# Kernel tuning notes

Hardware: AMD Instinct MI355X
Metric: run time of the kernel (lower is better)

The kernel has to match this reference:

```python
import jax, jax.numpy as jnp
import numpy as np
import math

B, N, DIM, H, DH, NNULL = 2, 2048, 1024, 16, 64, 2
SCALE = 8.0
LN_EPS = 1e-5


def _alibi_slopes(heads):
    # heads is a power of 2 here (16): slopes = start * start**i
    start = 2.0 ** (-(2.0 ** (-(math.log2(heads) - 3))))
    return np.array([start * (start ** i) for i in range(heads)], dtype=np.float32)


def setup_inputs() -> dict:
    key = jax.random.key(0)
    ks = jax.random.split(key, 6)
    inner = H * DH
    return {
        "x": jax.random.normal(ks[0], (B, N, DIM), dtype=jnp.float32),
        "norm_g": jnp.ones((DIM,), jnp.float32),
        "norm_b": jnp.zeros((DIM,), jnp.float32),
        "Wq": jax.random.normal(ks[1], (DIM, inner), jnp.float32) * 0.02,
        "Wkv": jax.random.normal(ks[2], (DIM, 2 * inner), jnp.float32) * 0.02,
        "q_scale": jnp.ones((DH,), jnp.float32),
        "k_scale": jnp.ones((DH,), jnp.float32),
        "null_kv": jax.random.normal(ks[3], (H, 2 * NNULL, DH), jnp.float32),
        "Wout": jax.random.normal(ks[4], (inner, DIM), jnp.float32) * 0.02,
    }


def _l2norm(t):
    # matches F.normalize: x / max(||x||, 1e-12)
    n = jnp.sqrt(jnp.sum(t * t, axis=-1, keepdims=True))
    return t / jnp.maximum(n, 1e-12)


def reference(x, norm_g, norm_b, Wq, Wkv, q_scale, k_scale, null_kv, Wout):
    b, n, dim = x.shape
    h, dh, nn = H, DH, NNULL
    j = n + nn

    # NOTE: faithful to source -- K/V come from the PRE-norm x (kv_input bound
    # before x = self.norm(x)); only Q uses the LayerNorm'd x.
    mu = jnp.mean(x, axis=-1, keepdims=True)
    var = jnp.mean((x - mu) ** 2, axis=-1, keepdims=True)
    xn = (x - mu) * jax.lax.rsqrt(var + LN_EPS) * norm_g + norm_b

    q = (xn @ Wq).reshape(b, n, h, dh).transpose(0, 2, 1, 3)          # b h n d
    kv = x @ Wkv
    k, v = jnp.split(kv, 2, axis=-1)
    k = k.reshape(b, n, h, dh).transpose(0, 2, 1, 3)                   # b h n d
    v = v.reshape(b, n, h, dh).transpose(0, 2, 1, 3)

    # null kv: (h, 2*nn, dh) -> (h, nn, 2, dh)
    null = null_kv.reshape(h, nn, 2, dh)
    nk = jnp.broadcast_to(null[:, :, 0, :][None], (b, h, nn, dh))
    nv = jnp.broadcast_to(null[:, :, 1, :][None], (b, h, nn, dh))
    k = jnp.concatenate([nk, k], axis=2)                               # b h j d
    v = jnp.concatenate([nv, v], axis=2)

    q = _l2norm(q) * q_scale
    k = _l2norm(k) * k_scale

    sim = jnp.einsum('bhid,bhjd->bhij', q, k) * SCALE                  # b h n j

    # ALiBi bias: rows at positions j-n..j-1, cols 0..j-1
    irow = jnp.arange(j - n, j)
    jcol = jnp.arange(j)
    bias = -jnp.abs(jcol[None, :] - irow[:, None]).astype(sim.dtype)   # (n, j)
    slopes = jnp.asarray(_alibi_slopes(h))[:, None, None]              # (h,1,1)
    sim = sim + slopes * bias

    # causal mask: triu with offset j - n + 1 (null kv always visible)
    causal = jnp.triu(jnp.ones((n, j), dtype=bool), k=j - n + 1)
    neg = jnp.finfo(sim.dtype).max
    sim = jnp.where(causal[None, None], -neg, sim)

    attn = jax.nn.softmax(sim, axis=-1)
    out = jnp.einsum('bhij,bhjd->bhid', attn, v)
    out = out.transpose(0, 2, 1, 3).reshape(b, n, h * dh)
    return out @ Wout
```

## Files before the change

### kernel.cpp

```cpp
#include <hip/hip_runtime.h>
#include <hip/hip_bf16.h>
#include <stdint.h>

#define H_    16
#define N_    2048
#define DIM_  1024
#define DH_   64
#define NN_   2
#define J_    2050
#define JP_   2112
#define B_    2
#define M_    4096
#define NSEG_ 84

#define S8L_  11.541560327111707f
#define LOG2E_ 1.4426950408889634f

typedef unsigned short u16;
typedef unsigned int u32;
typedef short bf16x8 __attribute__((ext_vector_type(8)));
typedef float f32x4 __attribute__((ext_vector_type(4)));

__device__ __forceinline__ u16 f2b(float f) {
  union { float f; unsigned int i; } v; v.f = f;
  unsigned int r = v.i + 0x7fffu + ((v.i >> 16) & 1u);
  return (u16)(r >> 16);
}
__device__ __forceinline__ float b2f(u16 u) {
  union { unsigned int i; float f; } v; v.i = ((unsigned int)u) << 16; return v.f;
}
__device__ __forceinline__ float lo2f(u32 u) {
  union { u32 i; float f; } v; v.i = u << 16; return v.f;
}
__device__ __forceinline__ float hi2f(u32 u) {
  union { u32 i; float f; } v; v.i = u & 0xffff0000u; return v.f;
}
__device__ __forceinline__ void unp8(const uint4 u, float* d) {
  d[0] = lo2f(u.x); d[1] = hi2f(u.x); d[2] = lo2f(u.y); d[3] = hi2f(u.y);
  d[4] = lo2f(u.z); d[5] = hi2f(u.z); d[6] = lo2f(u.w); d[7] = hi2f(u.w);
}
__device__ __forceinline__ u32 pk2(float a, float b) {
  union { __hip_bfloat162 h; u32 u; } x;
  x.h = __float22bfloat162_rn(make_float2(a, b));
  return x.u;
}
__device__ __forceinline__ void dma16(const u16* g, u16* l) {
  __builtin_amdgcn_global_load_lds(
      (const __attribute__((address_space(1))) u32*)(const void*)g,
      (__attribute__((address_space(3))) u32*)(void*)l, 16, 0, 0);
}

__global__ __launch_bounds__(256) void ktranspose3(const float* __restrict__ Wq,
                                                   const float* __restrict__ Wkv,
                                                   const float* __restrict__ Wout,
                                                   u16* __restrict__ WqT,
                                                   u16* __restrict__ WkvT,
                                                   u16* __restrict__ WoutT) {
  __shared__ float tile[32][33];
  int bx = blockIdx.x;
  const float* in; u16* out; int C; int cx;
  if (bx < 32)      { in = Wq;   out = WqT;   C = 1024; cx = bx; }
  else if (bx < 96) { in = Wkv;  out = WkvT;  C = 2048; cx = bx - 32; }
  else              { in = Wout; out = WoutT; C = 1024; cx = bx - 96; }
  const int R = 1024;
  int tx = threadIdx.x & 31, ty = threadIdx.x >> 5;
  int c0 = cx * 32, r0 = blockIdx.y * 32;
  #pragma unroll
  for (int i = 0; i < 32; i += 8)
    tile[ty + i][tx] = in[(size_t)(r0 + ty + i) * C + c0 + tx];
  __syncthreads();
  #pragma unroll
  for (int i = 0; i < 32; i += 8)
    out[(size_t)(c0 + ty + i) * R + r0 + tx] = f2b(tile[tx][ty + i]);
}

__global__ __launch_bounds__(256) void lnorm_k(const float* __restrict__ x,
                                               const float* __restrict__ g,
                                               const float* __restrict__ bb,
                                               u16* __restrict__ xn,
                                               u16* __restrict__ xbf) {
  int row = blockIdx.x;
  int t = threadIdx.x;
  float4 rw = *(const float4*)(x + (size_t)row * DIM_ + t * 4);
  float v0 = rw.x, v1 = rw.y, v2 = rw.z, v3 = rw.w;
  uint2 cw;
  cw.x = pk2(v0, v1);
  cw.y = pk2(v2, v3);
  *(uint2*)(xbf + (size_t)row * DIM_ + t * 4) = cw;
  float s = v0 + v1 + v2 + v3;
  float ss = v0 * v0 + v1 * v1 + v2 * v2 + v3 * v3;
  #pragma unroll
  for (int o = 32; o; o >>= 1) { s += __shfl_xor(s, o, 64); ss += __shfl_xor(ss, o, 64); }
  __shared__ float red[8];
  int lane = t & 63, w = t >> 6;
  if (lane == 0) { red[w] = s; red[4 + w] = ss; }
  __syncthreads();
  float S = red[0] + red[1] + red[2] + red[3];
  float SS = red[4] + red[5] + red[6] + red[7];
  float mu = S * (1.0f / DIM_);
  float var = SS * (1.0f / DIM_) - mu * mu;
  float rs = rsqrtf(var + 1e-5f);
  float4 gv = *(const float4*)(g + t * 4);
  float4 bv = *(const float4*)(bb + t * 4);
  uint2 ow;
  ow.x = pk2((v0 - mu) * rs * gv.x + bv.x, (v1 - mu) * rs * gv.y + bv.y);
  ow.y = pk2((v2 - mu) * rs * gv.z + bv.z, (v3 - mu) * rs * gv.w + bv.w);
  *(uint2*)(xn + (size_t)row * DIM_ + t * 4) = ow;
}

template <int MODE>
__global__ __launch_bounds__(256) void gemm_k(const u16* __restrict__ A,
                                              const u16* __restrict__ BT,
                                              void* __restrict__ dst0,
                                              void* __restrict__ dst1,
                                              const float* __restrict__ scale,
                                              int M, int Nc, int K) {
  __shared__ u16 As[2][128 * 64];
  __shared__ u16 Bs[2][64 * 64];
  int tid = threadIdx.x, wv = tid >> 6, lane = tid & 63;
  int fm = lane & 15, fg = lane >> 4;
  int nlin = (int)blockIdx.x + (int)gridDim.x * (int)blockIdx.y;
  int gx = (int)gridDim.x;
  int ypc = (int)gridDim.y >> 3;
  int mm = nlin >> 3;
  int row0 = ((nlin & 7) * ypc + mm / gx) * 128;
  int col0 = (mm % gx) * 64;
  f32x4 acc[2][4] = {};
  int srow = lane >> 3;
  int skb = ((lane & 7) ^ srow) * 8;
  const u16* Ag = A + (size_t)(row0 + wv * 32 + srow) * K + skb;
  const u16* Bg = BT + (size_t)(col0 + wv * 16 + srow) * K + skb;
  int fr7 = fm & 7;
  int ak0 = (fg ^ fr7) * 8;
  int ak1 = ((fg + 4) ^ fr7) * 8;
  {
    u16* AsW = As[0] + (wv * 32) * 64;
    u16* BsW = Bs[0] + (wv * 16) * 64;
    dma16(Ag,                    AsW);
    dma16(Ag + (size_t)8 * K,    AsW + 8 * 64);
    dma16(Ag + (size_t)16 * K,   AsW + 16 * 64);
    dma16(Ag + (size_t)24 * K,   AsW + 24 * 64);
    dma16(Bg,                    BsW);
    dma16(Bg + (size_t)8 * K,    BsW + 8 * 64);
  }
  __syncthreads();
  int cur = 0;
  for (int k0 = 0; k0 < K; k0 += 64) {
    if (k0 + 64 < K) {
      int kn = k0 + 64;
      u16* AsW = As[cur ^ 1] + (wv * 32) * 64;
      u16* BsW = Bs[cur ^ 1] + (wv * 16) * 64;
      dma16(Ag + kn,                    AsW);
      dma16(Ag + (size_t)8 * K + kn,    AsW + 8 * 64);
      dma16(Ag + (size_t)16 * K + kn,   AsW + 16 * 64);
      dma16(Ag + (size_t)24 * K + kn,   AsW + 24 * 64);
      dma16(Bg + kn,                    BsW);
      dma16(Bg + (size_t)8 * K + kn,    BsW + 8 * 64);
    }
    bf16x8 af0[2], af1[2], bf0[4], bf1[4];
    #pragma unroll
    for (int mt = 0; mt < 2; mt++) {
      int rbase = (wv * 32 + mt * 16 + fm) * 64;
      af0[mt] = *(const bf16x8*)&As[cur][rbase + ak0];
      af1[mt] = *(const bf16x8*)&As[cur][rbase + ak1];
    }
    #pragma unroll
    for (int nt = 0; nt < 4; nt++) {
      int rbase = (nt * 16 + fm) * 64;
      bf0[nt] = *(const bf16x8*)&Bs[cur][rbase + ak0];
      bf1[nt] = *(const bf16x8*)&Bs[cur][rbase + ak1];
    }
    #pragma unroll
    for (int mt = 0; mt < 2; mt++)
      #pragma unroll
      for (int nt = 0; nt < 4; nt++) {
        acc[mt][nt] = __builtin_amdgcn_mfma_f32_16x16x32_bf16(af0[mt], bf0[nt], acc[mt][nt], 0, 0, 0);
        acc[mt][nt] = __builtin_amdgcn_mfma_f32_16x16x32_bf16(af1[mt], bf1[nt], acc[mt][nt], 0, 0, 0);
      }
    __syncthreads();
    cur ^= 1;
  }
  if (MODE == 1) {
    float* C = (float*)dst0;
    #pragma unroll
    for (int mt = 0; mt < 2; mt++)
      #pragma unroll
      for (int r = 0; r < 4; r++) {
        int m = row0 + wv * 32 + mt * 16 + fg * 4 + r;
        #pragma unroll
        for (int nt = 0; nt < 4; nt++)
          C[(size_t)m * Nc + col0 + nt * 16 + fm] = acc[mt][nt][r];
      }
  } else {
    bool isK = (MODE == 2) || (col0 < 1024);
    int h = (isK ? col0 : col0 - 1024) >> 6;
    float sv[4];
    if (isK) {
      #pragma unroll
      for (int nt = 0; nt < 4; nt++) sv[nt] = scale[nt * 16 + fm];
      if (MODE == 2) {
        #pragma unroll
        for (int nt = 0; nt < 4; nt++) sv[nt] *= S8L_;
      }
    }
    u16* Do = (u16*)((MODE == 3 && !isK) ? dst1 : dst0);
    #pragma unroll
    for (int mt = 0; mt < 2; mt++) {
      #pragma unroll
      for (int r = 0; r < 4; r++) {
        float inv = 1.0f;
        if (isK) {
          float ssp = 0.0f;
          #pragma unroll
          for (int nt = 0; nt < 4; nt++) ssp += acc[mt][nt][r] * acc[mt][nt][r];
          #pragma unroll
          for (int o = 1; o <= 8; o <<= 1) ssp += __shfl_xor(ssp, o, 64);
          inv = 1.0f / fmaxf(sqrtf(ssp), 1e-12f);
        }
        int m = row0 + wv * 32 + mt * 16 + fg * 4 + r;
        int b = m >> 11, n = m & 2047;
        size_t base;
        if (MODE == 2)      base = (((size_t)(b * H_ + h)) * N_ + n) * 64;
        else if (isK)       base = (((size_t)(b * H_ + h)) * JP_ + (n + NN_)) * 64;
        else                base = (((size_t)(b * H_ + h)) * J_ + (n + NN_)) * 64;
        #pragma unroll
        for (int nt = 0; nt < 4; nt++) {
          float val = acc[mt][nt][r];
          if (isK) val = val * inv * sv[nt];
          Do[base + nt * 16 + fm] = f2b(val);
        }
      }
    }
  }
}

__global__ __launch_bounds__(256) void vtransp_k(const u16* __restrict__ Vb,
                                                 const float* __restrict__ nkv,
                                                 const float* __restrict__ ks,
                                                 u16* __restrict__ Kb,
                                                 u16* __restrict__ VTp) {
  __shared__ u16 tile[64][80];
  int t = threadIdx.x;
  int c = blockIdx.x, bh = blockIdx.y, h = bh & 15;
  int jl = t >> 2, dc = (t & 3) * 16;
  int j = c * 64 + jl;
  if (j < NN_) {
    float kvv[16];
    float kssp = 0.0f;
    #pragma unroll
    for (int e = 0; e < 16; e++) {
      float vv = nkv[(size_t)(h * 4 + 2 * j + 1) * 64 + dc + e];
      tile[jl][dc + e] = f2b(vv);
      float kv = nkv[(size_t)(h * 4 + 2 * j) * 64 + dc + e];
      kvv[e] = kv; kssp += kv * kv;
    }
    kssp += __shfl_xor(kssp, 1, 64);
    kssp += __shfl_xor(kssp, 2, 64);
    float inv = 1.0f / fmaxf(sqrtf(kssp), 1e-12f);
    #pragma unroll
    for (int e = 0; e < 16; e++)
      Kb[((size_t)bh * JP_ + j) * 64 + dc + e] = f2b(kvv[e] * inv * ks[dc + e]);
  } else if (j < J_) {
    const uint4* src = (const uint4*)(Vb + ((size_t)bh * J_ + j) * 64 + dc);
    *(uint4*)&tile[jl][dc] = src[0];
    *(uint4*)&tile[jl][dc + 8] = src[1];
  } else {
    uint4 z = {0, 0, 0, 0};
    *(uint4*)&tile[jl][dc] = z;
    *(uint4*)&tile[jl][dc + 8] = z;
    uint4* kd = (uint4*)(Kb + ((size_t)bh * JP_ + j) * 64 + dc);
    kd[0] = z;
    kd[1] = z;
  }
  __syncthreads();
  int d = t >> 2, p0 = (t & 3) * 16;
  u16 tmp[16] __attribute__((aligned(16)));
  #pragma unroll
  for (int e = 0; e < 16; e++) {
    int pos = p0 + e;
    int h2 = pos >> 5, rem = pos & 31;
    int fgp = rem >> 3, tt = rem & 7;
    int nt = tt >> 2, r = tt & 3;
    int jloc = (h2 * 2 + nt) * 16 + fgp * 4 + r;
    tmp[e] = tile[jloc][d];
  }
  uint4* dstp = (uint4*)(VTp + ((size_t)bh * 64 + d) * JP_ + c * 64 + p0);
  dstp[0] = ((uint4*)tmp)[0];
  dstp[1] = ((uint4*)tmp)[1];
}

__global__ __launch_bounds__(256, 6) void attn_k(const u16* __restrict__ Qn,
                                                 const u16* __restrict__ Kb,
                                                 const u16* __restrict__ VTp,
                                                 const float* __restrict__ qs,
                                                 const float* __restrict__ ks,
                                                 u16* __restrict__ partials) {
  __shared__ u16 Ks0[64 * 32], Ks1[64 * 32];
  __shared__ u16 Vs0[64 * 32], Vs1[64 * 32];
  int tid = threadIdx.x;
  int wv = tid >> 6, lane = tid & 63;
  int fm = lane & 15, fg = lane >> 4;
  int n = (int)blockIdx.x + NSEG_ * (int)blockIdx.y;
  int m = n >> 3;
  int bh = (n & 7) * 4 + m / NSEG_;
  int segid = m % NSEG_;
  int h = bh & 15;
  int cum = 0, qt = 0, seg = 0;
  #pragma unroll 1
  for (int i = 0; i < 32; i++) {
    int t = 31 - i, s = (t + 9) >> 3;
    if (segid < cum + s) { qt = t; seg = segid - cum; break; }
    cum += s;
  }
  int q0 = qt * 64;
  int q = q0 + wv * 16 + fm;
  float slope = exp2f(-0.5f * (float)(h + 1));
  float prod = fabsf(qs[lane] * ks[lane]);
  #pragma unroll
  for (int o = 32; o; o >>= 1) prod = fmaxf(prod, __shfl_xor(prod, o, 64));
  float MbL = 8.0f * prod * LOG2E_;
  float slopeL = slope * LOG2E_;
  const u16* qp = Qn + ((size_t)bh * N_ + q) * 64 + fg * 8;
  bf16x8 qf0 = *(const bf16x8*)(qp);
  bf16x8 qf1 = *(const bf16x8*)(qp + 32);
  f32x4 accO[4] = {};
  float lp = 0.0f;
  int lr = lane >> 2;
  int kbs = ((lane & 3) ^ ((lane >> 3) & 3)) * 8;
  int fs = (fg ^ ((fm >> 1) & 3)) * 8;
  const u16* KbBH = Kb + (size_t)bh * JP_ * 64;
  const u16* VTbh = VTp + (size_t)bh * 64 * JP_;
  int c0 = seg * 8;
  int c1 = min(c0 + 8, qt + 2);
  float bias0 = slopeL * (float)(c0 * 64 + fg * 4 - q - 2) - MbL;
  float sr1 = slopeL, sr2 = slopeL * 2.0f, sr3 = slopeL * 3.0f;
  float s16 = slopeL * 16.0f;
  float d64 = slopeL * 64.0f;
  for (int c = c0; c < c1; c++) {
    int jb = c * 64;
    __syncthreads();
    const u16* Kg = KbBH + (size_t)(jb + wv * 16 + lr) * 64 + kbs;
    dma16(Kg,      Ks0 + wv * 512);
    dma16(Kg + 32, Ks1 + wv * 512);
    const u16* Vg = VTbh + (size_t)(wv * 16 + lr) * JP_ + jb + kbs;
    dma16(Vg,      Vs0 + wv * 512);
    dma16(Vg + 32, Vs1 + wv * 512);
    __syncthreads();
    f32x4 accS[4] = {};
    #pragma unroll
    for (int nt = 0; nt < 4; nt++) {
      bf16x8 kf0 = *(const bf16x8*)&Ks0[(nt * 16 + fm) * 32 + fs];
      accS[nt] = __builtin_amdgcn_mfma_f32_16x16x32_bf16(kf0, qf0, accS[nt], 0, 0, 0);
      bf16x8 kf1 = *(const bf16x8*)&Ks1[(nt * 16 + fm) * 32 + fs];
      accS[nt] = __builtin_amdgcn_mfma_f32_16x16x32_bf16(kf1, qf1, accS[nt], 0, 0, 0);
    }
    union { bf16x8 v; u32 u[4]; } P0, P1;
    float lps = 0.0f;
    float bnt = bias0;
    if (c < qt) {
      #pragma unroll
      for (int nt = 0; nt < 4; nt++) {
        float e0 = __builtin_amdgcn_exp2f(accS[nt][0] + bnt);
        float e1 = __builtin_amdgcn_exp2f((accS[nt][1] + sr1) + bnt);
        float e2 = __builtin_amdgcn_exp2f((accS[nt][2] + sr2) + bnt);
        float e3 = __builtin_amdgcn_exp2f((accS[nt][3] + sr3) + bnt);
        u32 w0 = pk2(e0, e1);
        u32 w1 = pk2(e2, e3);
        lps += (e0 + e1) + (e2 + e3);
        if (nt < 2) { P0.u[nt * 2] = w0; P0.u[nt * 2 + 1] = w1; }
        else        { P1.u[(nt - 2) * 2] = w0; P1.u[(nt - 2) * 2 + 1] = w1; }
        bnt += s16;
      }
    } else {
      int thr = q + 2 - jb;
      #pragma unroll
      for (int nt = 0; nt < 4; nt++) {
        int ib = nt * 16 + fg * 4;
        float e0 = __builtin_amdgcn_exp2f(accS[nt][0] + bnt);
        float e1 = __builtin_amdgcn_exp2f((accS[nt][1] + sr1) + bnt);
        float e2 = __builtin_amdgcn_exp2f((accS[nt][2] + sr2) + bnt);
        float e3 = __builtin_amdgcn_exp2f((accS[nt][3] + sr3) + bnt);
        e0 = (ib + 0 <= thr) ? e0 : 0.0f;
        e1 = (ib + 1 <= thr) ? e1 : 0.0f;
        e2 = (ib + 2 <= thr) ? e2 : 0.0f;
        e3 = (ib + 3 <= thr) ? e3 : 0.0f;
        u32 w0 = pk2(e0, e1);
        u32 w1 = pk2(e2, e3);
        lps += (e0 + e1) + (e2 + e3);
        if (nt < 2) { P0.u[nt * 2] = w0; P0.u[nt * 2 + 1] = w1; }
        else        { P1.u[(nt - 2) * 2] = w0; P1.u[(nt - 2) * 2 + 1] = w1; }
        bnt += s16;
      }
    }
    lp += lps;
    bias0 += d64;
    #pragma unroll
    for (int nt = 0; nt < 4; nt++) {
      bf16x8 vf0 = *(const bf16x8*)&Vs0[(nt * 16 + fm) * 32 + fs];
      accO[nt] = __builtin_amdgcn_mfma_f32_16x16x32_bf16(vf0, P0.v, accO[nt], 0, 0, 0);
      bf16x8 vf1 = *(const bf16x8*)&Vs1[(nt * 16 + fm) * 32 + fs];
      accO[nt] = __builtin_amdgcn_mfma_f32_16x16x32_bf16(vf1, P1.v, accO[nt], 0, 0, 0);
    }
  }
  lp += __shfl_xor(lp, 16, 64);
  lp += __shfl_xor(lp, 32, 64);
  u16* P = partials + ((size_t)bh * NSEG_ + segid) * 4224;
  int sq = wv * 16 + fm;
  #pragma unroll
  for (int nt = 0; nt < 4; nt++) {
    uint2 ow;
    ow.x = pk2(accO[nt][0], accO[nt][1]);
    ow.y = pk2(accO[nt][2], accO[nt][3]);
    *(uint2*)(P + sq * 64 + nt * 16 + fg * 4) = ow;
  }
  if (fg == 0) *(float*)(P + 4096 + 2 * sq) = lp;
}

__global__ __launch_bounds__(256) void comb_k(const u16* __restrict__ partials,
                                              u16* __restrict__ AO) {
  int qt = blockIdx.x, bh = blockIdx.y, b = bh >> 4, h = bh & 15;
  int t = threadIdx.x, q = t >> 2, dq = (t & 3) * 16;
  int s = (qt + 9) >> 3;
  int cum = 0;
  for (int tt = qt + 1; tt < 32; tt++) cum += (tt + 9) >> 3;
  float acc[16] = {};
  float lsum = 0.0f;
  for (int k = 0; k < s; k++) {
    const u16* P = partials + ((size_t)bh * NSEG_ + cum + k) * 4224;
    uint4 a = *(const uint4*)(P + q * 64 + dq);
    uint4 bq = *(const uint4*)(P + q * 64 + dq + 8);
    float tmp[8];
    unp8(a, tmp);
    #pragma unroll
    for (int e = 0; e < 8; e++) acc[e] += tmp[e];
    unp8(bq, tmp);
    #pragma unroll
    for (int e = 0; e < 8; e++) acc[8 + e] += tmp[e];
    lsum += *(const float*)(P + 4096 + 2 * q);
  }
  float linv = 1.0f / lsum;
  int n = qt * 64 + q;
  u16* dst = AO + (((size_t)(b * N_ + n)) * H_ + h) * 64 + dq;
  u16 ov[16] __attribute__((aligned(16)));
  #pragma unroll
  for (int e = 0; e < 16; e++) ov[e] = f2b(acc[e] * linv);
  *(uint4*)dst = ((uint4*)ov)[0];
  *(uint4*)(dst + 8) = ((uint4*)ov)[1];
}

extern "C" void kernel_launch(void* const* d_in, const int* in_sizes, int n_in,
                              void* d_out, int out_size, void* d_ws, size_t ws_size,
                              hipStream_t stream) {
  const float* x    = (const float*)d_in[0];
  const float* ng   = (const float*)d_in[1];
  const float* nb   = (const float*)d_in[2];
  const float* Wq   = (const float*)d_in[3];
  const float* Wkv  = (const float*)d_in[4];
  const float* qs   = (const float*)d_in[5];
  const float* ks   = (const float*)d_in[6];
  const float* nkv  = (const float*)d_in[7];
  const float* Wout = (const float*)d_in[8];
  float* out = (float*)d_out;
  char* ws = (char*)d_ws;

  u16* xn    = (u16*)(ws + 0);
  u16* WoutT = (u16*)(ws + 8388608);
  u16* Qn    = (u16*)(ws + 10485760);
  u16* Kb    = (u16*)(ws + 18874368);
  u16* VTp   = (u16*)(ws + 27525120);
  u16* xbf   = (u16*)(ws + 36175872);
  u16* WqT   = (u16*)(ws + 44564480);
  u16* WkvT  = (u16*)(ws + 46661632);
  u16* Vb    = (u16*)(ws + 50855936);
  u16* parts = xbf;
  u16* AO    = xn;

  ktranspose3<<<dim3(128, 32), 256, 0, stream>>>(Wq, Wkv, Wout, WqT, WkvT, WoutT);
  lnorm_k<<<4096, 256, 0, stream>>>(x, ng, nb, xn, xbf);
  gemm_k<2><<<dim3(16, 32), 256, 0, stream>>>(xn, WqT, Qn, nullptr, qs, M_, 1024, 1024);
  gemm_k<3><<<dim3(32, 32), 256, 0, stream>>>(xbf, WkvT, Kb, Vb, ks, M_, 2048, 1024);
  vtransp_k<<<dim3(33, 32), 256, 0, stream>>>(Vb, nkv, ks, Kb, VTp);
  attn_k<<<dim3(NSEG_, 32), 256, 0, stream>>>(Qn, Kb, VTp, qs, ks, parts);
  comb_k<<<dim3(32, 32), 256, 0, stream>>>(parts, AO);
  gemm_k<1><<<dim3(16, 32), 256, 0, stream>>>(AO, WoutT, out, nullptr, nullptr, M_, 1024, 1024);
}
```

Before: 214.4 us.

## Double query tile per attention block to 128 rows, reusing K/V fragments

Each wave now processes 32 query rows (two 16-row MFMA tiles) instead of 16, so every K/V tile loaded into shared memory and every K/V fragment read from LDS feeds twice as many MFMAs. Segments are re-split into 9-chunk pieces over 128-row query tiles, and the partial-combine kernel is updated to the new slot layout. Waves whose rows lie entirely above the causal diagonal of a chunk skip compute. The cost is roughly doubled accumulator registers (occupancy hint lowered from 6 to 4), fewer blocks for load balance, and more masked work on the diagonal.

```diff
diff --git a/kernel.cpp b/kernel.cpp
--- a/kernel.cpp
+++ b/kernel.cpp
@@ -11,7 +11,9 @@
 #define JP_   2112
 #define B_    2
 #define M_    4096
-#define NSEG_ 84
+#define QT2_  16
+#define NSEG2_ 39
+#define SLOT2_ 8448
 
 #define S8L_  11.541560327111707f
 #define LOG2E_ 1.4426950408889634f
@@ -25,9 +27,6 @@
   union { float f; unsigned int i; } v; v.f = f;
   unsigned int r = v.i + 0x7fffu + ((v.i >> 16) & 1u);
   return (u16)(r >> 16);
-}
-__device__ __forceinline__ float b2f(u16 u) {
-  union { unsigned int i; float f; } v; v.i = ((unsigned int)u) << 16; return v.f;
 }
 __device__ __forceinline__ float lo2f(u32 u) {
   union { u32 i; float f; } v; v.i = u << 16; return v.f;
@@ -289,7 +288,44 @@
   dstp[1] = ((uint4*)tmp)[1];
 }
 
-__global__ __launch_bounds__(256, 6) void attn_k(const u16* __restrict__ Qn,
+#define SOFTMAX16(ACCS, BSTART, FULLVIS, THR, LP, PW)                                \
+  {                                                                                  \
+    float bnt = (BSTART);                                                            \
+    float lps = 0.0f;                                                                \
+    if (FULLVIS) {                                                                   \
+      _Pragma("unroll")                                                              \
+      for (int nt = 0; nt < 4; nt++) {                                               \
+        float e0 = __builtin_amdgcn_exp2f(ACCS[nt][0] + bnt);                        \
+        float e1 = __builtin_amdgcn_exp2f((ACCS[nt][1] + sr1) + bnt);                \
+        float e2 = __builtin_amdgcn_exp2f((ACCS[nt][2] + sr2) + bnt);                \
+        float e3 = __builtin_amdgcn_exp2f((ACCS[nt][3] + sr3) + bnt);                \
+        PW[nt * 2] = pk2(e0, e1);                                                    \
+        PW[nt * 2 + 1] = pk2(e2, e3);                                                \
+        lps += (e0 + e1) + (e2 + e3);                                                \
+        bnt += s16;                                                                  \
+      }                                                                              \
+    } else {                                                                         \
+      _Pragma("unroll")                                                              \
+      for (int nt = 0; nt < 4; nt++) {                                               \
+        int ib = nt * 16 + fg4;                                                      \
+        float e0 = __builtin_amdgcn_exp2f(ACCS[nt][0] + bnt);                        \
+        float e1 = __builtin_amdgcn_exp2f((ACCS[nt][1] + sr1) + bnt);                \
+        float e2 = __builtin_amdgcn_exp2f((ACCS[nt][2] + sr2) + bnt);                \
+        float e3 = __builtin_amdgcn_exp2f((ACCS[nt][3] + sr3) + bnt);                \
+        e0 = (ib + 0 <= (THR)) ? e0 : 0.0f;                                          \
+        e1 = (ib + 1 <= (THR)) ? e1 : 0.0f;                                          \
+        e2 = (ib + 2 <= (THR)) ? e2 : 0.0f;                                          \
+        e3 = (ib + 3 <= (THR)) ? e3 : 0.0f;                                          \
+        PW[nt * 2] = pk2(e0, e1);                                                    \
+        PW[nt * 2 + 1] = pk2(e2, e3);                                                \
+        lps += (e0 + e1) + (e2 + e3);                                                \
+        bnt += s16;                                                                  \
+      }                                                                              \
+    }                                                                                \
+    LP += lps;                                                                       \
+  }
+
+__global__ __launch_bounds__(256, 4) void attn_k(const u16* __restrict__ Qn,
                                                  const u16* __restrict__ Kb,
                                                  const u16* __restrict__ VTp,
                                                  const float* __restrict__ qs,
@@ -300,39 +336,43 @@
   int tid = threadIdx.x;
   int wv = tid >> 6, lane = tid & 63;
   int fm = lane & 15, fg = lane >> 4;
-  int n = (int)blockIdx.x + NSEG_ * (int)blockIdx.y;
+  int fg4 = fg * 4;
+  int n = (int)blockIdx.x + NSEG2_ * (int)blockIdx.y;
   int m = n >> 3;
-  int bh = (n & 7) * 4 + m / NSEG_;
-  int segid = m % NSEG_;
+  int bh = (n & 7) * 4 + m / NSEG2_;
+  int segid = m % NSEG2_;
   int h = bh & 15;
-  int cum = 0, qt = 0, seg = 0;
+  int cum = 0, qt2 = 0, seg = 0;
   #pragma unroll 1
-  for (int i = 0; i < 32; i++) {
-    int t = 31 - i, s = (t + 9) >> 3;
-    if (segid < cum + s) { qt = t; seg = segid - cum; break; }
+  for (int i = 0; i < 16; i++) {
+    int t = 15 - i, s = (2 * t + 11) / 9;
+    if (segid < cum + s) { qt2 = t; seg = segid - cum; break; }
     cum += s;
   }
-  int q0 = qt * 64;
-  int q = q0 + wv * 16 + fm;
+  int q0 = qt2 * 128;
+  int qw = q0 + wv * 32;
+  int qr = qw + fm;
   float slope = exp2f(-0.5f * (float)(h + 1));
   float prod = fabsf(qs[lane] * ks[lane]);
   #pragma unroll
   for (int o = 32; o; o >>= 1) prod = fmaxf(prod, __shfl_xor(prod, o, 64));
   float MbL = 8.0f * prod * LOG2E_;
   float slopeL = slope * LOG2E_;
-  const u16* qp = Qn + ((size_t)bh * N_ + q) * 64 + fg * 8;
-  bf16x8 qf0 = *(const bf16x8*)(qp);
-  bf16x8 qf1 = *(const bf16x8*)(qp + 32);
-  f32x4 accO[4] = {};
-  float lp = 0.0f;
+  const u16* qp = Qn + ((size_t)bh * N_ + qr) * 64 + fg * 8;
+  bf16x8 qa0 = *(const bf16x8*)(qp);
+  bf16x8 qa1 = *(const bf16x8*)(qp + 32);
+  bf16x8 qb0 = *(const bf16x8*)(qp + 16 * 64);
+  bf16x8 qb1 = *(const bf16x8*)(qp + 16 * 64 + 32);
+  f32x4 accO[2][4] = {};
+  float lp0 = 0.0f, lp1 = 0.0f;
   int lr = lane >> 2;
   int kbs = ((lane & 3) ^ ((lane >> 3) & 3)) * 8;
   int fs = (fg ^ ((fm >> 1) & 3)) * 8;
   const u16* KbBH = Kb + (size_t)bh * JP_ * 64;
   const u16* VTbh = VTp + (size_t)bh * 64 * JP_;
-  int c0 = seg * 8;
-  int c1 = min(c0 + 8, qt + 2);
-  float bias0 = slopeL * (float)(c0 * 64 + fg * 4 - q - 2) - MbL;
+  int c0 = seg * 9;
+  int c1 = min(c0 + 9, 2 * qt2 + 3);
+  float bias0 = slopeL * (float)(c0 * 64 + fg4 - qr - 2) - MbL;
   float sr1 = slopeL, sr2 = slopeL * 2.0f, sr3 = slopeL * 3.0f;
   float s16 = slopeL * 16.0f;
   float d64 = slopeL * 64.0f;
@@ -346,106 +386,84 @@
     dma16(Vg,      Vs0 + wv * 512);
     dma16(Vg + 32, Vs1 + wv * 512);
     __syncthreads();
-    f32x4 accS[4] = {};
+    if (jb <= qw + 33) {
+      f32x4 accS0[4] = {}, accS1[4] = {};
+      #pragma unroll
+      for (int nt = 0; nt < 4; nt++) {
+        bf16x8 kf0 = *(const bf16x8*)&Ks0[(nt * 16 + fm) * 32 + fs];
+        accS0[nt] = __builtin_amdgcn_mfma_f32_16x16x32_bf16(kf0, qa0, accS0[nt], 0, 0, 0);
+        accS1[nt] = __builtin_amdgcn_mfma_f32_16x16x32_bf16(kf0, qb0, accS1[nt], 0, 0, 0);
+        bf16x8 kf1 = *(const bf16x8*)&Ks1[(nt * 16 + fm) * 32 + fs];
+        accS0[nt] = __builtin_amdgcn_mfma_f32_16x16x32_bf16(kf1, qa1, accS0[nt], 0, 0, 0);
+        accS1[nt] = __builtin_amdgcn_mfma_f32_16x16x32_bf16(kf1, qb1, accS1[nt], 0, 0, 0);
+      }
+      union { bf16x8 v[2]; u32 u[8]; } PA, PB;
+      bool fv0 = (jb + 61 <= qw);
+      bool fv1 = (jb + 61 <= qw + 16);
+      int thr0 = qr + 2 - jb;
+      SOFTMAX16(accS0, bias0, fv0, thr0, lp0, PA.u);
+      SOFTMAX16(accS1, bias0 - s16, fv1, thr0 + 16, lp1, PB.u);
+      #pragma unroll
+      for (int nt = 0; nt < 4; nt++) {
+        bf16x8 vf0 = *(const bf16x8*)&Vs0[(nt * 16 + fm) * 32 + fs];
+        accO[0][nt] = __builtin_amdgcn_mfma_f32_16x16x32_bf16(vf0, PA.v[0], accO[0][nt], 0, 0, 0);
+        accO[1][nt] = __builtin_amdgcn_mfma_f32_16x16x32_bf16(vf0, PB.v[0], accO[1][nt], 0, 0, 0);
+        bf16x8 vf1 = *(const bf16x8*)&Vs1[(nt * 16 + fm) * 32 + fs];
+        accO[0][nt] = __builtin_amdgcn_mfma_f32_16x16x32_bf16(vf1, PA.v[1], accO[0][nt], 0, 0, 0);
+        accO[1][nt] = __builtin_amdgcn_mfma_f32_16x16x32_bf16(vf1, PB.v[1], accO[1][nt], 0, 0, 0);
+      }
+    }
+    bias0 += d64;
+  }
+  lp0 += __shfl_xor(lp0, 16, 64);
+  lp0 += __shfl_xor(lp0, 32, 64);
+  lp1 += __shfl_xor(lp1, 16, 64);
+  lp1 += __shfl_xor(lp1, 32, 64);
+  u16* P = partials + ((size_t)bh * NSEG2_ + segid) * SLOT2_;
+  #pragma unroll
+  for (int mt = 0; mt < 2; mt++) {
+    int sq = wv * 32 + mt * 16 + fm;
     #pragma unroll
     for (int nt = 0; nt < 4; nt++) {
-      bf16x8 kf0 = *(const bf16x8*)&Ks0[(nt * 16 + fm) * 32 + fs];
-      accS[nt] = __builtin_amdgcn_mfma_f32_16x16x32_bf16(kf0, qf0, accS[nt], 0, 0, 0);
-      bf16x8 kf1 = *(const bf16x8*)&Ks1[(nt * 16 + fm) * 32 + fs];
-      accS[nt] = __builtin_amdgcn_mfma_f32_16x16x32_bf16(kf1, qf1, accS[nt], 0, 0, 0);
-    }
-    union { bf16x8 v; u32 u[4]; } P0, P1;
-    float lps = 0.0f;
-    float bnt = bias0;
-    if (c < qt) {
-      #pragma unroll
-      for (int nt = 0; nt < 4; nt++) {
-        float e0 = __builtin_amdgcn_exp2f(accS[nt][0] + bnt);
-        float e1 = __builtin_amdgcn_exp2f((accS[nt][1] + sr1) + bnt);
-        float e2 = __builtin_amdgcn_exp2f((accS[nt][2] + sr2) + bnt);
-        float e3 = __builtin_amdgcn_exp2f((accS[nt][3] + sr3) + bnt);
-        u32 w0 = pk2(e0, e1);
-        u32 w1 = pk2(e2, e3);
-        lps += (e0 + e1) + (e2 + e3);
-        if (nt < 2) { P0.u[nt * 2] = w0; P0.u[nt * 2 + 1] = w1; }
-        else        { P1.u[(nt - 2) * 2] = w0; P1.u[(nt - 2) * 2 + 1] = w1; }
-        bnt += s16;
-      }
-    } else {
-      int thr = q + 2 - jb;
-      #pragma unroll
-      for (int nt = 0; nt < 4; nt++) {
-        int ib = nt * 16 + fg * 4;
-        float e0 = __builtin_amdgcn_exp2f(accS[nt][0] + bnt);
-        float e1 = __builtin_amdgcn_exp2f((accS[nt][1] + sr1) + bnt);
-        float e2 = __builtin_amdgcn_exp2f((accS[nt][2] + sr2) + bnt);
-        float e3 = __builtin_amdgcn_exp2f((accS[nt][3] + sr3) + bnt);
-        e0 = (ib + 0 <= thr) ? e0 : 0.0f;
-        e1 = (ib + 1 <= thr) ? e1 : 0.0f;
-        e2 = (ib + 2 <= thr) ? e2 : 0.0f;
-        e3 = (ib + 3 <= thr) ? e3 : 0.0f;
-        u32 w0 = pk2(e0, e1);
-        u32 w1 = pk2(e2, e3);
-        lps += (e0 + e1) + (e2 + e3);
-        if (nt < 2) { P0.u[nt * 2] = w0; P0.u[nt * 2 + 1] = w1; }
-        else        { P1.u[(nt - 2) * 2] = w0; P1.u[(nt - 2) * 2 + 1] = w1; }
-        bnt += s16;
-      }
-    }
-    lp += lps;
-    bias0 += d64;
-    #pragma unroll
-    for (int nt = 0; nt < 4; nt++) {
-      bf16x8 vf0 = *(const bf16x8*)&Vs0[(nt * 16 + fm) * 32 + fs];
-      accO[nt] = __builtin_amdgcn_mfma_f32_16x16x32_bf16(vf0, P0.v, accO[nt], 0, 0, 0);
-      bf16x8 vf1 = *(const bf16x8*)&Vs1[(nt * 16 + fm) * 32 + fs];
-      accO[nt] = __builtin_amdgcn_mfma_f32_16x16x32_bf16(vf1, P1.v, accO[nt], 0, 0, 0);
-    }
-  }
-  lp += __shfl_xor(lp, 16, 64);
-  lp += __shfl_xor(lp, 32, 64);
-  u16* P = partials + ((size_t)bh * NSEG_ + segid) * 4224;
-  int sq = wv * 16 + fm;
-  #pragma unroll
-  for (int nt = 0; nt < 4; nt++) {
-    uint2 ow;
-    ow.x = pk2(accO[nt][0], accO[nt][1]);
-    ow.y = pk2(accO[nt][2], accO[nt][3]);
-    *(uint2*)(P + sq * 64 + nt * 16 + fg * 4) = ow;
-  }
-  if (fg == 0) *(float*)(P + 4096 + 2 * sq) = lp;
+      uint2 ow;
+      ow.x = pk2(accO[mt][nt][0], accO[mt][nt][1]);
+      ow.y = pk2(accO[mt][nt][2], accO[mt][nt][3]);
+      *(uint2*)(P + sq * 64 + nt * 16 + fg4) = ow;
+    }
+    if (fg == 0) *(float*)(P + 8192 + 2 * sq) = (mt == 0) ? lp0 : lp1;
+  }
 }
 
 __global__ __launch_bounds__(256) void comb_k(const u16* __restrict__ partials,
                                               u16* __restrict__ AO) {
-  int qt = blockIdx.x, bh = blockIdx.y, b = bh >> 4, h = bh & 15;
-  int t = threadIdx.x, q = t >> 2, dq = (t & 3) * 16;
-  int s = (qt + 9) >> 3;
+  int qt2 = blockIdx.x, bh = blockIdx.y, b = bh >> 4, h = bh & 15;
+  int t = threadIdx.x, q = t >> 1, dh = (t & 1) * 32;
+  int s = (2 * qt2 + 11) / 9;
   int cum = 0;
-  for (int tt = qt + 1; tt < 32; tt++) cum += (tt + 9) >> 3;
-  float acc[16] = {};
+  for (int tt = qt2 + 1; tt < 16; tt++) cum += (2 * tt + 11) / 9;
+  float acc[32] = {};
   float lsum = 0.0f;
   for (int k = 0; k < s; k++) {
-    const u16* P = partials + ((size_t)bh * NSEG_ + cum + k) * 4224;
-    uint4 a = *(const uint4*)(P + q * 64 + dq);
-    uint4 bq = *(const uint4*)(P + q * 64 + dq + 8);
+    const u16* P = partials + ((size_t)bh * NSEG2_ + cum + k) * SLOT2_;
     float tmp[8];
-    unp8(a, tmp);
-    #pragma unroll
-    for (int e = 0; e < 8; e++) acc[e] += tmp[e];
-    unp8(bq, tmp);
-    #pragma unroll
-    for (int e = 0; e < 8; e++) acc[8 + e] += tmp[e];
-    lsum += *(const float*)(P + 4096 + 2 * q);
+    #pragma unroll
+    for (int w = 0; w < 4; w++) {
+      uint4 a = *(const uint4*)(P + q * 64 + dh + w * 8);
+      unp8(a, tmp);
+      #pragma unroll
+      for (int e = 0; e < 8; e++) acc[w * 8 + e] += tmp[e];
+    }
+    lsum += *(const float*)(P + 8192 + 2 * q);
   }
   float linv = 1.0f / lsum;
-  int n = qt * 64 + q;
-  u16* dst = AO + (((size_t)(b * N_ + n)) * H_ + h) * 64 + dq;
-  u16 ov[16] __attribute__((aligned(16)));
-  #pragma unroll
-  for (int e = 0; e < 16; e++) ov[e] = f2b(acc[e] * linv);
-  *(uint4*)dst = ((uint4*)ov)[0];
-  *(uint4*)(dst + 8) = ((uint4*)ov)[1];
+  int nrow = qt2 * 128 + q;
+  u16* dst = AO + (((size_t)(b * N_ + nrow)) * H_ + h) * 64 + dh;
+  u16 ov[32] __attribute__((aligned(16)));
+  #pragma unroll
+  for (int e = 0; e < 32; e++) ov[e] = f2b(acc[e] * linv);
+  #pragma unroll
+  for (int w = 0; w < 4; w++)
+    *(uint4*)(dst + w * 8) = ((uint4*)ov)[w];
 }
 
 extern "C" void kernel_launch(void* const* d_in, const int* in_sizes, int n_in,
@@ -480,7 +498,7 @@
   gemm_k<2><<<dim3(16, 32), 256, 0, stream>>>(xn, WqT, Qn, nullptr, qs, M_, 1024, 1024);
   gemm_k<3><<<dim3(32, 32), 256, 0, stream>>>(xbf, WkvT, Kb, Vb, ks, M_, 2048, 1024);
   vtransp_k<<<dim3(33, 32), 256, 0, stream>>>(Vb, nkv, ks, Kb, VTp);
-  attn_k<<<dim3(NSEG_, 32), 256, 0, stream>>>(Qn, Kb, VTp, qs, ks, parts);
-  comb_k<<<dim3(32, 32), 256, 0, stream>>>(parts, AO);
+  attn_k<<<dim3(NSEG2_, 32), 256, 0, stream>>>(Qn, Kb, VTp, qs, ks, parts);
+  comb_k<<<dim3(16, 32), 256, 0, stream>>>(parts, AO);
   gemm_k<1><<<dim3(16, 32), 256, 0, stream>>>(AO, WoutT, out, nullptr, nullptr, M_, 1024, 1024);
 }
```

After: 213.4 us. About the same (-0.5%).

## Fuse prep kernels, widen GEMM tiles to 128x128, write V transposed from GEMM

Applied to the files above, without the earlier changes.

Merges the weight transpose, LayerNorm and null-KV/padding setup into one prep kernel. The GEMM tile grows from 128x64 to 128x128 using a 2x2 wave layout with 4x4 MFMA tiles per wave. The KV GEMM epilogue now writes V straight into the permuted transposed layout, which removes the separate vtransp kernel and the Vb buffer. This cuts launches and intermediate traffic but raises register and LDS use per block and halves the GEMM grid. The V stores are also scattered, with stride JP_ between adjacent lanes.

```diff
diff --git a/kernel.cpp b/kernel.cpp
--- a/kernel.cpp
+++ b/kernel.cpp
@@ -26,9 +26,6 @@
   unsigned int r = v.i + 0x7fffu + ((v.i >> 16) & 1u);
   return (u16)(r >> 16);
 }
-__device__ __forceinline__ float b2f(u16 u) {
-  union { unsigned int i; float f; } v; v.i = ((unsigned int)u) << 16; return v.f;
-}
 __device__ __forceinline__ float lo2f(u32 u) {
   union { u32 i; float f; } v; v.i = u << 16; return v.f;
 }
@@ -50,62 +47,93 @@
       (__attribute__((address_space(3))) u32*)(void*)l, 16, 0, 0);
 }
 
-__global__ __launch_bounds__(256) void ktranspose3(const float* __restrict__ Wq,
-                                                   const float* __restrict__ Wkv,
-                                                   const float* __restrict__ Wout,
-                                                   u16* __restrict__ WqT,
-                                                   u16* __restrict__ WkvT,
-                                                   u16* __restrict__ WoutT) {
+__global__ __launch_bounds__(256) void prep_k(const float* __restrict__ x,
+                                              const float* __restrict__ g,
+                                              const float* __restrict__ bb,
+                                              const float* __restrict__ Wq,
+                                              const float* __restrict__ Wkv,
+                                              const float* __restrict__ Wout,
+                                              const float* __restrict__ nkv,
+                                              const float* __restrict__ ks,
+                                              u16* __restrict__ xn,
+                                              u16* __restrict__ xbf,
+                                              u16* __restrict__ WqT,
+                                              u16* __restrict__ WkvT,
+                                              u16* __restrict__ WoutT,
+                                              u16* __restrict__ Kb,
+                                              u16* __restrict__ VTp) {
   __shared__ float tile[32][33];
-  int bx = blockIdx.x;
-  const float* in; u16* out; int C; int cx;
-  if (bx < 32)      { in = Wq;   out = WqT;   C = 1024; cx = bx; }
-  else if (bx < 96) { in = Wkv;  out = WkvT;  C = 2048; cx = bx - 32; }
-  else              { in = Wout; out = WoutT; C = 1024; cx = bx - 96; }
-  const int R = 1024;
-  int tx = threadIdx.x & 31, ty = threadIdx.x >> 5;
-  int c0 = cx * 32, r0 = blockIdx.y * 32;
-  #pragma unroll
-  for (int i = 0; i < 32; i += 8)
-    tile[ty + i][tx] = in[(size_t)(r0 + ty + i) * C + c0 + tx];
-  __syncthreads();
-  #pragma unroll
-  for (int i = 0; i < 32; i += 8)
-    out[(size_t)(c0 + ty + i) * R + r0 + tx] = f2b(tile[tx][ty + i]);
-}
-
-__global__ __launch_bounds__(256) void lnorm_k(const float* __restrict__ x,
-                                               const float* __restrict__ g,
-                                               const float* __restrict__ bb,
-                                               u16* __restrict__ xn,
-                                               u16* __restrict__ xbf) {
-  int row = blockIdx.x;
+  __shared__ float red[8];
+  int bx = blockIdx.x, by = blockIdx.y;
   int t = threadIdx.x;
-  float4 rw = *(const float4*)(x + (size_t)row * DIM_ + t * 4);
-  float v0 = rw.x, v1 = rw.y, v2 = rw.z, v3 = rw.w;
-  uint2 cw;
-  cw.x = pk2(v0, v1);
-  cw.y = pk2(v2, v3);
-  *(uint2*)(xbf + (size_t)row * DIM_ + t * 4) = cw;
-  float s = v0 + v1 + v2 + v3;
-  float ss = v0 * v0 + v1 * v1 + v2 * v2 + v3 * v3;
-  #pragma unroll
-  for (int o = 32; o; o >>= 1) { s += __shfl_xor(s, o, 64); ss += __shfl_xor(ss, o, 64); }
-  __shared__ float red[8];
-  int lane = t & 63, w = t >> 6;
-  if (lane == 0) { red[w] = s; red[4 + w] = ss; }
-  __syncthreads();
-  float S = red[0] + red[1] + red[2] + red[3];
-  float SS = red[4] + red[5] + red[6] + red[7];
-  float mu = S * (1.0f / DIM_);
-  float var = SS * (1.0f / DIM_) - mu * mu;
-  float rs = rsqrtf(var + 1e-5f);
-  float4 gv = *(const float4*)(g + t * 4);
-  float4 bv = *(const float4*)(bb + t * 4);
-  uint2 ow;
-  ow.x = pk2((v0 - mu) * rs * gv.x + bv.x, (v1 - mu) * rs * gv.y + bv.y);
-  ow.y = pk2((v2 - mu) * rs * gv.z + bv.z, (v3 - mu) * rs * gv.w + bv.w);
-  *(uint2*)(xn + (size_t)row * DIM_ + t * 4) = ow;
+  if (bx < 128) {
+    const float* in; u16* out; int C; int cx;
+    if (bx < 32)      { in = Wq;   out = WqT;   C = 1024; cx = bx; }
+    else if (bx < 96) { in = Wkv;  out = WkvT;  C = 2048; cx = bx - 32; }
+    else              { in = Wout; out = WoutT; C = 1024; cx = bx - 96; }
+    const int R = 1024;
+    int tx = t & 31, ty = t >> 5;
+    int c0 = cx * 32, r0 = by * 32;
+    #pragma unroll
+    for (int i = 0; i < 32; i += 8)
+      tile[ty + i][tx] = in[(size_t)(r0 + ty + i) * C + c0 + tx];
+    __syncthreads();
+    #pragma unroll
+    for (int i = 0; i < 32; i += 8)
+      out[(size_t)(c0 + ty + i) * R + r0 + tx] = f2b(tile[tx][ty + i]);
+  } else if (bx < 256) {
+    int row = (bx - 128) * 32 + by;
+    float4 rw = *(const float4*)(x + (size_t)row * DIM_ + t * 4);
+    float v0 = rw.x, v1 = rw.y, v2 = rw.z, v3 = rw.w;
+    uint2 cw;
+    cw.x = pk2(v0, v1);
+    cw.y = pk2(v2, v3);
+    *(uint2*)(xbf + (size_t)row * DIM_ + t * 4) = cw;
+    float s = v0 + v1 + v2 + v3;
+    float ss = v0 * v0 + v1 * v1 + v2 * v2 + v3 * v3;
+    #pragma unroll
+    for (int o = 32; o; o >>= 1) { s += __shfl_xor(s, o, 64); ss += __shfl_xor(ss, o, 64); }
+    int lane = t & 63, w = t >> 6;
+    if (lane == 0) { red[w] = s; red[4 + w] = ss; }
+    __syncthreads();
+    float S = red[0] + red[1] + red[2] + red[3];
+    float SS = red[4] + red[5] + red[6] + red[7];
+    float mu = S * (1.0f / DIM_);
+    float var = SS * (1.0f / DIM_) - mu * mu;
+    float rs = rsqrtf(var + 1e-5f);
+    float4 gv = *(const float4*)(g + t * 4);
+    float4 bv = *(const float4*)(bb + t * 4);
+    uint2 ow;
+    ow.x = pk2((v0 - mu) * rs * gv.x + bv.x, (v1 - mu) * rs * gv.y + bv.y);
+    ow.y = pk2((v2 - mu) * rs * gv.z + bv.z, (v3 - mu) * rs * gv.w + bv.w);
+    *(uint2*)(xn + (size_t)row * DIM_ + t * 4) = ow;
+  } else if (bx == 256) {
+    int bh = by, h = bh & 15;
+    if (t < 128) {
+      int j = t >> 6, d = t & 63;
+      float kv = nkv[(size_t)(h * 4 + 2 * j) * 64 + d];
+      float vv = nkv[(size_t)(h * 4 + 2 * j + 1) * 64 + d];
+      float ssp = kv * kv;
+      #pragma unroll
+      for (int o = 32; o; o >>= 1) ssp += __shfl_xor(ssp, o, 64);
+      float inv = 1.0f / fmaxf(sqrtf(ssp), 1e-12f);
+      Kb[((size_t)bh * JP_ + j) * 64 + d] = f2b(kv * inv * ks[d]);
+      VTp[((size_t)bh * 64 + d) * JP_ + j] = f2b(vv);
+    }
+  } else if (bx == 257) {
+    int bh = by;
+    uint4 z = {0, 0, 0, 0};
+    u16* dst = Kb + ((size_t)bh * JP_ + 2048) * 64 + t * 16;
+    ((uint4*)dst)[0] = z;
+    ((uint4*)dst)[1] = z;
+  } else {
+    int bh = by;
+    uint4 z = {0, 0, 0, 0};
+    int d = t >> 2, p0 = (t & 3) * 16;
+    u16* dst = VTp + ((size_t)bh * 64 + d) * JP_ + 2048 + p0;
+    ((uint4*)dst)[0] = z;
+    ((uint4*)dst)[1] = z;
+  }
 }
 
 template <int MODE>
@@ -116,62 +144,57 @@
                                               const float* __restrict__ scale,
                                               int M, int Nc, int K) {
   __shared__ u16 As[2][128 * 64];
-  __shared__ u16 Bs[2][64 * 64];
+  __shared__ u16 Bs[2][128 * 64];
   int tid = threadIdx.x, wv = tid >> 6, lane = tid & 63;
   int fm = lane & 15, fg = lane >> 4;
+  int fg4 = fg * 4;
+  int wr = wv >> 1, wc = wv & 1;
   int nlin = (int)blockIdx.x + (int)gridDim.x * (int)blockIdx.y;
   int gx = (int)gridDim.x;
   int ypc = (int)gridDim.y >> 3;
   int mm = nlin >> 3;
   int row0 = ((nlin & 7) * ypc + mm / gx) * 128;
-  int col0 = (mm % gx) * 64;
-  f32x4 acc[2][4] = {};
+  int col0 = (mm % gx) * 128;
+  f32x4 acc[4][4] = {};
   int srow = lane >> 3;
   int skb = ((lane & 7) ^ srow) * 8;
   const u16* Ag = A + (size_t)(row0 + wv * 32 + srow) * K + skb;
-  const u16* Bg = BT + (size_t)(col0 + wv * 16 + srow) * K + skb;
+  const u16* Bg = BT + (size_t)(col0 + wv * 32 + srow) * K + skb;
   int fr7 = fm & 7;
   int ak0 = (fg ^ fr7) * 8;
   int ak1 = ((fg + 4) ^ fr7) * 8;
-  {
-    u16* AsW = As[0] + (wv * 32) * 64;
-    u16* BsW = Bs[0] + (wv * 16) * 64;
-    dma16(Ag,                    AsW);
-    dma16(Ag + (size_t)8 * K,    AsW + 8 * 64);
-    dma16(Ag + (size_t)16 * K,   AsW + 16 * 64);
-    dma16(Ag + (size_t)24 * K,   AsW + 24 * 64);
-    dma16(Bg,                    BsW);
-    dma16(Bg + (size_t)8 * K,    BsW + 8 * 64);
-  }
+  auto stageg = [&](int k0, int buf) {
+    u16* AsW = As[buf] + (wv * 32) * 64;
+    u16* BsW = Bs[buf] + (wv * 32) * 64;
+    dma16(Ag + k0,                    AsW);
+    dma16(Ag + (size_t)8 * K + k0,    AsW + 8 * 64);
+    dma16(Ag + (size_t)16 * K + k0,   AsW + 16 * 64);
+    dma16(Ag + (size_t)24 * K + k0,   AsW + 24 * 64);
+    dma16(Bg + k0,                    BsW);
+    dma16(Bg + (size_t)8 * K + k0,    BsW + 8 * 64);
+    dma16(Bg + (size_t)16 * K + k0,   BsW + 16 * 64);
+    dma16(Bg + (size_t)24 * K + k0,   BsW + 24 * 64);
+  };
+  stageg(0, 0);
   __syncthreads();
   int cur = 0;
   for (int k0 = 0; k0 < K; k0 += 64) {
-    if (k0 + 64 < K) {
-      int kn = k0 + 64;
-      u16* AsW = As[cur ^ 1] + (wv * 32) * 64;
-      u16* BsW = Bs[cur ^ 1] + (wv * 16) * 64;
-      dma16(Ag + kn,                    AsW);
-      dma16(Ag + (size_t)8 * K + kn,    AsW + 8 * 64);
-      dma16(Ag + (size_t)16 * K + kn,   AsW + 16 * 64);
-      dma16(Ag + (size_t)24 * K + kn,   AsW + 24 * 64);
-      dma16(Bg + kn,                    BsW);
-      dma16(Bg + (size_t)8 * K + kn,    BsW + 8 * 64);
-    }
-    bf16x8 af0[2], af1[2], bf0[4], bf1[4];
-    #pragma unroll
-    for (int mt = 0; mt < 2; mt++) {
-      int rbase = (wv * 32 + mt * 16 + fm) * 64;
+    if (k0 + 64 < K) stageg(k0 + 64, cur ^ 1);
+    bf16x8 af0[4], af1[4], bf0[4], bf1[4];
+    #pragma unroll
+    for (int mt = 0; mt < 4; mt++) {
+      int rbase = (wr * 64 + mt * 16 + fm) * 64;
       af0[mt] = *(const bf16x8*)&As[cur][rbase + ak0];
       af1[mt] = *(const bf16x8*)&As[cur][rbase + ak1];
     }
     #pragma unroll
     for (int nt = 0; nt < 4; nt++) {
-      int rbase = (nt * 16 + fm) * 64;
+      int rbase = (wc * 64 + nt * 16 + fm) * 64;
       bf0[nt] = *(const bf16x8*)&Bs[cur][rbase + ak0];
       bf1[nt] = *(const bf16x8*)&Bs[cur][rbase + ak1];
     }
     #pragma unroll
-    for (int mt = 0; mt < 2; mt++)
+    for (int mt = 0; mt < 4; mt++)
       #pragma unroll
       for (int nt = 0; nt < 4; nt++) {
         acc[mt][nt] = __builtin_amdgcn_mfma_f32_16x16x32_bf16(af0[mt], bf0[nt], acc[mt][nt], 0, 0, 0);
@@ -180,113 +203,71 @@
     __syncthreads();
     cur ^= 1;
   }
+  int colw = col0 + wc * 64;
   if (MODE == 1) {
     float* C = (float*)dst0;
     #pragma unroll
-    for (int mt = 0; mt < 2; mt++)
+    for (int mt = 0; mt < 4; mt++)
       #pragma unroll
       for (int r = 0; r < 4; r++) {
-        int m = row0 + wv * 32 + mt * 16 + fg * 4 + r;
+        int m = row0 + wr * 64 + mt * 16 + fg4 + r;
         #pragma unroll
         for (int nt = 0; nt < 4; nt++)
-          C[(size_t)m * Nc + col0 + nt * 16 + fm] = acc[mt][nt][r];
+          C[(size_t)m * Nc + colw + nt * 16 + fm] = acc[mt][nt][r];
       }
   } else {
-    bool isK = (MODE == 2) || (col0 < 1024);
-    int h = (isK ? col0 : col0 - 1024) >> 6;
-    float sv[4];
+    bool isK = (MODE == 2) || (colw < 1024);
+    int h = (isK ? colw : colw - 1024) >> 6;
     if (isK) {
+      float sv[4];
       #pragma unroll
       for (int nt = 0; nt < 4; nt++) sv[nt] = scale[nt * 16 + fm];
       if (MODE == 2) {
         #pragma unroll
         for (int nt = 0; nt < 4; nt++) sv[nt] *= S8L_;
       }
-    }
-    u16* Do = (u16*)((MODE == 3 && !isK) ? dst1 : dst0);
-    #pragma unroll
-    for (int mt = 0; mt < 2; mt++) {
-      #pragma unroll
-      for (int r = 0; r < 4; r++) {
-        float inv = 1.0f;
-        if (isK) {
+      u16* Do = (u16*)dst0;
+      #pragma unroll
+      for (int mt = 0; mt < 4; mt++) {
+        #pragma unroll
+        for (int r = 0; r < 4; r++) {
           float ssp = 0.0f;
           #pragma unroll
           for (int nt = 0; nt < 4; nt++) ssp += acc[mt][nt][r] * acc[mt][nt][r];
           #pragma unroll
           for (int o = 1; o <= 8; o <<= 1) ssp += __shfl_xor(ssp, o, 64);
-          inv = 1.0f / fmaxf(sqrtf(ssp), 1e-12f);
+          float inv = 1.0f / fmaxf(sqrtf(ssp), 1e-12f);
+          int m = row0 + wr * 64 + mt * 16 + fg4 + r;
+          int b = m >> 11, n = m & 2047;
+          size_t base;
+          if (MODE == 2) base = (((size_t)(b * H_ + h)) * N_ + n) * 64;
+          else           base = (((size_t)(b * H_ + h)) * JP_ + (n + NN_)) * 64;
+          #pragma unroll
+          for (int nt = 0; nt < 4; nt++)
+            Do[base + nt * 16 + fm] = f2b(acc[mt][nt][r] * inv * sv[nt]);
         }
-        int m = row0 + wv * 32 + mt * 16 + fg * 4 + r;
-        int b = m >> 11, n = m & 2047;
-        size_t base;
-        if (MODE == 2)      base = (((size_t)(b * H_ + h)) * N_ + n) * 64;
-        else if (isK)       base = (((size_t)(b * H_ + h)) * JP_ + (n + NN_)) * 64;
-        else                base = (((size_t)(b * H_ + h)) * J_ + (n + NN_)) * 64;
+      }
+    } else {
+      u16* Do = (u16*)dst1;
+      #pragma unroll
+      for (int mt = 0; mt < 4; mt++) {
         #pragma unroll
-        for (int nt = 0; nt < 4; nt++) {
-          float val = acc[mt][nt][r];
-          if (isK) val = val * inv * sv[nt];
-          Do[base + nt * 16 + fm] = f2b(val);
+        for (int r = 0; r < 4; r++) {
+          int m = row0 + wr * 64 + mt * 16 + fg4 + r;
+          int b = m >> 11, n = m & 2047;
+          int j = n + NN_;
+          int c2 = j >> 6, jl = j & 63;
+          int rem = jl & 31;
+          int pos = (jl >> 5) * 32 + ((rem >> 2) & 3) * 8 + (rem >> 4) * 4 + (rem & 3);
+          size_t hb = (size_t)(b * H_ + h) * 64;
+          int off = c2 * 64 + pos;
+          #pragma unroll
+          for (int nt = 0; nt < 4; nt++)
+            Do[(hb + nt * 16 + fm) * JP_ + off] = f2b(acc[mt][nt][r]);
         }
       }
     }
   }
-}
-
-__global__ __launch_bounds__(256) void vtransp_k(const u16* __restrict__ Vb,
-                                                 const float* __restrict__ nkv,
-                                                 const float* __restrict__ ks,
-                                                 u16* __restrict__ Kb,
-                                                 u16* __restrict__ VTp) {
-  __shared__ u16 tile[64][80];
-  int t = threadIdx.x;
-  int c = blockIdx.x, bh = blockIdx.y, h = bh & 15;
-  int jl = t >> 2, dc = (t & 3) * 16;
-  int j = c * 64 + jl;
-  if (j < NN_) {
-    float kvv[16];
-    float kssp = 0.0f;
-    #pragma unroll
-    for (int e = 0; e < 16; e++) {
-      float vv = nkv[(size_t)(h * 4 + 2 * j + 1) * 64 + dc + e];
-      tile[jl][dc + e] = f2b(vv);
-      float kv = nkv[(size_t)(h * 4 + 2 * j) * 64 + dc + e];
-      kvv[e] = kv; kssp += kv * kv;
-    }
-    kssp += __shfl_xor(kssp, 1, 64);
-    kssp += __shfl_xor(kssp, 2, 64);
-    float inv = 1.0f / fmaxf(sqrtf(kssp), 1e-12f);
-    #pragma unroll
-    for (int e = 0; e < 16; e++)
-      Kb[((size_t)bh * JP_ + j) * 64 + dc + e] = f2b(kvv[e] * inv * ks[dc + e]);
-  } else if (j < J_) {
-    const uint4* src = (const uint4*)(Vb + ((size_t)bh * J_ + j) * 64 + dc);
-    *(uint4*)&tile[jl][dc] = src[0];
-    *(uint4*)&tile[jl][dc + 8] = src[1];
-  } else {
-    uint4 z = {0, 0, 0, 0};
-    *(uint4*)&tile[jl][dc] = z;
-    *(uint4*)&tile[jl][dc + 8] = z;
-    uint4* kd = (uint4*)(Kb + ((size_t)bh * JP_ + j) * 64 + dc);
-    kd[0] = z;
-    kd[1] = z;
-  }
-  __syncthreads();
-  int d = t >> 2, p0 = (t & 3) * 16;
-  u16 tmp[16] __attribute__((aligned(16)));
-  #pragma unroll
-  for (int e = 0; e < 16; e++) {
-    int pos = p0 + e;
-    int h2 = pos >> 5, rem = pos & 31;
-    int fgp = rem >> 3, tt = rem & 7;
-    int nt = tt >> 2, r = tt & 3;
-    int jloc = (h2 * 2 + nt) * 16 + fgp * 4 + r;
-    tmp[e] = tile[jloc][d];
-  }
-  uint4* dstp = (uint4*)(VTp + ((size_t)bh * 64 + d) * JP_ + c * 64 + p0);
-  dstp[0] = ((uint4*)tmp)[0];
-  dstp[1] = ((uint4*)tmp)[1];
 }
 
 __global__ __launch_bounds__(256, 6) void attn_k(const u16* __restrict__ Qn,
@@ -471,16 +452,14 @@
   u16* xbf   = (u16*)(ws + 36175872);
   u16* WqT   = (u16*)(ws + 44564480);
   u16* WkvT  = (u16*)(ws + 46661632);
-  u16* Vb    = (u16*)(ws + 50855936);
   u16* parts = xbf;
   u16* AO    = xn;
 
-  ktranspose3<<<dim3(128, 32), 256, 0, stream>>>(Wq, Wkv, Wout, WqT, WkvT, WoutT);
-  lnorm_k<<<4096, 256, 0, stream>>>(x, ng, nb, xn, xbf);
-  gemm_k<2><<<dim3(16, 32), 256, 0, stream>>>(xn, WqT, Qn, nullptr, qs, M_, 1024, 1024);
-  gemm_k<3><<<dim3(32, 32), 256, 0, stream>>>(xbf, WkvT, Kb, Vb, ks, M_, 2048, 1024);
-  vtransp_k<<<dim3(33, 32), 256, 0, stream>>>(Vb, nkv, ks, Kb, VTp);
+  prep_k<<<dim3(259, 32), 256, 0, stream>>>(x, ng, nb, Wq, Wkv, Wout, nkv, ks,
+                                            xn, xbf, WqT, WkvT, WoutT, Kb, VTp);
+  gemm_k<2><<<dim3(8, 32), 256, 0, stream>>>(xn, WqT, Qn, nullptr, qs, M_, 1024, 1024);
+  gemm_k<3><<<dim3(16, 32), 256, 0, stream>>>(xbf, WkvT, Kb, VTp, ks, M_, 2048, 1024);
   attn_k<<<dim3(NSEG_, 32), 256, 0, stream>>>(Qn, Kb, VTp, qs, ks, parts);
   comb_k<<<dim3(32, 32), 256, 0, stream>>>(parts, AO);
-  gemm_k<1><<<dim3(16, 32), 256, 0, stream>>>(AO, WoutT, out, nullptr, nullptr, M_, 1024, 1024);
-}
+  gemm_k<1><<<dim3(8, 32), 256, 0, stream>>>(AO, WoutT, out, nullptr, nullptr, M_, 1024, 1024);
+}
```

Result: no change. 211.5 us (-1.4%).
